# Kernel optimization log

Hardware: AMD Instinct MI355X
Metric: run time of the kernel (lower is better)

## Reference

```python
import jax, jax.numpy as jnp
import numpy as np

N = 100000            # number of pose-graph nodes (keyframes)
E = 2000000           # number of edges (last one is the 'key' edge)
KEY_EDGE_WEIGHT = 0.1 # default key_edge_weight in forward
_EPS2 = 1e-8          # small-angle threshold on squared norms
_TINY = 1e-12

# quaternion layout follows pypose: [x, y, z, w]; SE3 7-vec is [t(3), q(4)]

def _quat_to_mat(q):
    x, y, z, w = q[..., 0], q[..., 1], q[..., 2], q[..., 3]
    xx, yy, zz = x * x, y * y, z * z
    xy, xz, yz = x * y, x * z, y * z
    wx, wy, wz = w * x, w * y, w * z
    R = jnp.stack([
        jnp.stack([1 - 2 * (yy + zz), 2 * (xy - wz), 2 * (xz + wy)], -1),
        jnp.stack([2 * (xy + wz), 1 - 2 * (xx + zz), 2 * (yz - wx)], -1),
        jnp.stack([2 * (xz - wy), 2 * (yz + wx), 1 - 2 * (xx + yy)], -1),
    ], -2)
    return R  # [...,3,3]

def _mat_to_tq(M):
    """mat2SE3: [...,4,4] -> (t [...,3], q [...,4] xyzw). Branchless copysign method."""
    R = M[..., :3, :3]
    t = M[..., :3, 3]
    m00, m11, m22 = R[..., 0, 0], R[..., 1, 1], R[..., 2, 2]
    qw = 0.5 * jnp.sqrt(jnp.clip(1 + m00 + m11 + m22, _TINY))
    sx = jnp.where(R[..., 2, 1] - R[..., 1, 2] >= 0, 1.0, -1.0)
    sy = jnp.where(R[..., 0, 2] - R[..., 2, 0] >= 0, 1.0, -1.0)
    sz = jnp.where(R[..., 1, 0] - R[..., 0, 1] >= 0, 1.0, -1.0)
    qx = sx * 0.5 * jnp.sqrt(jnp.clip(1 + m00 - m11 - m22, _TINY))
    qy = sy * 0.5 * jnp.sqrt(jnp.clip(1 - m00 + m11 - m22, _TINY))
    qz = sz * 0.5 * jnp.sqrt(jnp.clip(1 - m00 - m11 + m22, _TINY))
    return t, jnp.stack([qx, qy, qz, qw], -1)

def _qmul(q1, q2):
    v1, w1 = q1[..., :3], q1[..., 3:]
    v2, w2 = q2[..., :3], q2[..., 3:]
    w = w1 * w2 - jnp.sum(v1 * v2, -1, keepdims=True)
    v = w1 * v2 + w2 * v1 + jnp.cross(v1, v2)
    return jnp.concatenate([v, w], -1)

def _qrot(q, v):
    qv, w = q[..., :3], q[..., 3:]
    return v + 2.0 * jnp.cross(qv, jnp.cross(qv, v) + w * v)

def _so3_log(q):
    """unit quaternion -> rotation vector phi [...,3]."""
    s = jnp.where(q[..., 3:] < 0, -1.0, 1.0)  # canonical hemisphere (w>=0)
    v, w = s * q[..., :3], (s * q[..., 3:])[..., 0]
    n2 = jnp.sum(v * v, -1)
    n = jnp.sqrt(jnp.clip(n2, _TINY))
    big = 2.0 * jnp.arctan2(n, w) / n
    small = 2.0 / w - 2.0 * n2 / (3.0 * w ** 3)
    scale = jnp.where(n2 > _EPS2, big, small)
    return scale[..., None] * v

def _se3_log(t, q):
    """SE3 Log map -> [tau(3), phi(3)] (pypose se3 ordering)."""
    phi = _so3_log(q)
    th2 = jnp.sum(phi * phi, -1)
    th = jnp.sqrt(jnp.clip(th2, _TINY))
    half = 0.5 * th
    sin_half = jnp.where(th2 > _EPS2, jnp.sin(half), 1.0)
    coef_big = (1.0 - half * jnp.cos(half) / sin_half) / jnp.clip(th2, _TINY)
    coef = jnp.where(th2 > _EPS2, coef_big, 1.0 / 12.0 + th2 / 720.0)
    pxt = jnp.cross(phi, t)
    tau = t - 0.5 * pxt + coef[..., None] * jnp.cross(phi, pxt)
    return jnp.concatenate([tau, phi], -1)

def setup_inputs() -> dict:
    key = jax.random.key(0)
    k1, k2, k3, k4, k5 = jax.random.split(key, 5)
    # node SE3 params: random unit quats + translations -> [N,7]
    qn = jax.random.normal(k1, (N, 4), jnp.float32)
    qn = qn / jnp.linalg.norm(qn, axis=-1, keepdims=True)
    tn = jax.random.normal(k2, (N, 3), jnp.float32)
    nodes = jnp.concatenate([tn, qn], -1)
    edges = jax.random.randint(k3, (E, 2), 0, N, dtype=jnp.int64)
    # measurement poses as valid 4x4 SE3 matrices [E,4,4]
    qe = jax.random.normal(k4, (E, 4), jnp.float32)
    qe = qe / jnp.linalg.norm(qe, axis=-1, keepdims=True)
    te = jax.random.normal(k5, (E, 3), jnp.float32)
    top = jnp.concatenate([_quat_to_mat(qe), te[..., None]], -1)   # [E,3,4]
    bottom = jnp.broadcast_to(jnp.array([0.0, 0.0, 0.0, 1.0], jnp.float32), (E, 1, 4))
    poses = jnp.concatenate([top, bottom], -2)
    return {"nodes": nodes, "poses": poses, "edges": edges}

def reference(nodes, poses, edges):
    # nodes_all = cat([poses_SE3[0:1] (frozen), nodes[1:]])
    nodes_all = jnp.concatenate([jax.lax.stop_gradient(nodes[:1]), nodes[1:]], 0)
    n1 = nodes_all[edges[:, 0]]
    n2 = nodes_all[edges[:, 1]]
    t1, q1 = n1[:, :3], n1[:, 3:]
    t2, q2 = n2[:, :3], n2[:, 3:]
    # rel = node1.Inv() @ node2
    q1i = jnp.concatenate([-q1[:, :3], q1[:, 3:]], -1)
    t12 = _qrot(q1i, t2 - t1)
    q12 = _qmul(q1i, q2)
    # error = mat2SE3(poses) @ rel
    tp, qp = _mat_to_tq(poses)
    te_ = tp + _qrot(qp, t12)
    qe_ = _qmul(qp, q12)
    err = _se3_log(te_, qe_)  # [E,6]
    # last edge is the key edge, scaled by key_edge_weight (same math as the
    # original's split-then-concat, done with one vectorized pass + row weight)
    w = jnp.concatenate([jnp.ones((E - 1,), err.dtype),
                         jnp.full((1,), KEY_EDGE_WEIGHT, err.dtype)])
    return err * w[:, None]
```

## Files before the change

kernel.cpp:

```cpp
#include <hip/hip_runtime.h>

#define K_EPS2 1e-8f
#define K_TINY 1e-12f
#define KEY_EDGE_WEIGHT 0.1f

__device__ __forceinline__ float3 f3(float x, float y, float z) { return make_float3(x, y, z); }
__device__ __forceinline__ float3 add3(float3 a, float3 b) { return f3(a.x + b.x, a.y + b.y, a.z + b.z); }
__device__ __forceinline__ float3 sub3(float3 a, float3 b) { return f3(a.x - b.x, a.y - b.y, a.z - b.z); }
__device__ __forceinline__ float3 scl3(float s, float3 a) { return f3(s * a.x, s * a.y, s * a.z); }
__device__ __forceinline__ float dot3(float3 a, float3 b) { return a.x * b.x + a.y * b.y + a.z * b.z; }
__device__ __forceinline__ float3 cross3(float3 a, float3 b) {
    return f3(a.y * b.z - a.z * b.y,
              a.z * b.x - a.x * b.z,
              a.x * b.y - a.y * b.x);
}

__device__ __forceinline__ float3 qrot(float3 qv, float qw, float3 v) {
    float3 t = add3(cross3(qv, v), scl3(qw, v));
    return add3(v, scl3(2.0f, cross3(qv, t)));
}

__device__ __forceinline__ void qmul(float3 v1, float w1, float3 v2, float w2,
                                     float3* v, float* w) {
    *w = w1 * w2 - dot3(v1, v2);
    *v = add3(add3(scl3(w1, v2), scl3(w2, v1)), cross3(v1, v2));
}

__global__ __launch_bounds__(256) void PoseGraph_kernel(
    const float* __restrict__ nodes,
    const float* __restrict__ poses,
    const int*   __restrict__ edges,
    float*       __restrict__ out,
    int E) {
    int e = blockIdx.x * blockDim.x + threadIdx.x;
    if (e >= E) return;

    int2 ij = *(const int2*)(edges + (size_t)2 * e);

    const float* pn1 = nodes + (size_t)ij.x * 7;
    const float* pn2 = nodes + (size_t)ij.y * 7;
    float3 t1  = f3(pn1[0], pn1[1], pn1[2]);
    float3 q1v = f3(pn1[3], pn1[4], pn1[5]);
    float  q1w = pn1[6];
    float3 t2  = f3(pn2[0], pn2[1], pn2[2]);
    float3 q2v = f3(pn2[3], pn2[4], pn2[5]);
    float  q2w = pn2[6];

    float3 q1iv = f3(-q1v.x, -q1v.y, -q1v.z);
    float3 t12 = qrot(q1iv, q1w, sub3(t2, t1));
    float3 q12v; float q12w;
    qmul(q1iv, q1w, q2v, q2w, &q12v, &q12w);

    const float4* p4 = (const float4*)(poses + (size_t)e * 16);
    float4 r0 = p4[0];
    float4 r1 = p4[1];
    float4 r2 = p4[2];
    float m00 = r0.x, m01 = r0.y, m02 = r0.z;
    float m10 = r1.x, m11 = r1.y, m12 = r1.z;
    float m20 = r2.x, m21 = r2.y, m22 = r2.z;
    float3 tp = f3(r0.w, r1.w, r2.w);

    float qpw = 0.5f * sqrtf(fmaxf(1.0f + m00 + m11 + m22, K_TINY));
    float qpx = ((m21 - m12 >= 0.0f) ? 0.5f : -0.5f) * sqrtf(fmaxf(1.0f + m00 - m11 - m22, K_TINY));
    float qpy = ((m02 - m20 >= 0.0f) ? 0.5f : -0.5f) * sqrtf(fmaxf(1.0f - m00 + m11 - m22, K_TINY));
    float qpz = ((m10 - m01 >= 0.0f) ? 0.5f : -0.5f) * sqrtf(fmaxf(1.0f - m00 - m11 + m22, K_TINY));
    float3 qpv = f3(qpx, qpy, qpz);

    float3 te = add3(tp, qrot(qpv, qpw, t12));
    float3 qev; float qew;
    qmul(qpv, qpw, q12v, q12w, &qev, &qew);

    float s = (qew < 0.0f) ? -1.0f : 1.0f;
    float3 v = scl3(s, qev);
    float w = s * qew;
    float nn2 = dot3(v, v);
    float scale;
    if (nn2 > K_EPS2) {
        float n = sqrtf(nn2);
        scale = 2.0f * atan2f(n, w) / n;
    } else {
        scale = 2.0f / w - 2.0f * nn2 / (3.0f * w * w * w);
    }
    float3 phi = scl3(scale, v);

    float th2 = dot3(phi, phi);
    float coef;
    if (th2 > K_EPS2) {
        float th = sqrtf(th2);
        float half = 0.5f * th;
        float sh = sinf(half);
        float ch = cosf(half);
        coef = (1.0f - half * ch / sh) / th2;
    } else {
        coef = 1.0f / 12.0f + th2 / 720.0f;
    }
    float3 pxt = cross3(phi, te);
    float3 tau = add3(sub3(te, scl3(0.5f, pxt)), scl3(coef, cross3(phi, pxt)));

    float wgt = (e == E - 1) ? KEY_EDGE_WEIGHT : 1.0f;

    float* o = out + (size_t)e * 6;
    *(float2*)(o + 0) = make_float2(tau.x * wgt, tau.y * wgt);
    *(float2*)(o + 2) = make_float2(tau.z * wgt, phi.x * wgt);
    *(float2*)(o + 4) = make_float2(phi.y * wgt, phi.z * wgt);
}

extern "C" void kernel_launch(void* const* d_in, const int* in_sizes, int n_in,
                              void* d_out, int out_size, void* d_ws, size_t ws_size,
                              hipStream_t stream) {
    const float* nodes = (const float*)d_in[0];
    const float* poses = (const float*)d_in[1];
    const int*   edges = (const int*)d_in[2];
    float* out = (float*)d_out;

    int E = in_sizes[2] / 2;
    int threads = 256;
    int blocks = (E + threads - 1) / threads;
    PoseGraph_kernel<<<blocks, threads, 0, stream>>>(nodes, poses, edges, out, E);
}
```

Before: 53.48 us.

## Repack node poses to 32-byte aligned rows and use nontemporal streaming accesses

Adds a pre-pass kernel that copies the 7-float node array into an 8-float padded workspace, so each gathered node can be read with two aligned 16-byte loads instead of seven scalar loads. Edge indices and pose matrices are now read, and outputs written, with nontemporal hints so streaming data does not evict the reused node table from cache. The cost is an extra kernel launch and a pass over the nodes each call. The packed path only runs when the workspace is large enough; otherwise the original layout is used.

Result: slower. 71.46 us (+33.6%).

```diff
diff --git a/kernel.cpp b/kernel.cpp
--- a/kernel.cpp
+++ b/kernel.cpp
@@ -3,6 +3,10 @@
 #define K_EPS2 1e-8f
 #define K_TINY 1e-12f
 #define KEY_EDGE_WEIGHT 0.1f
+
+typedef float  vf4 __attribute__((ext_vector_type(4)));
+typedef float  vf2 __attribute__((ext_vector_type(2)));
+typedef int    vi2 __attribute__((ext_vector_type(2)));
 
 __device__ __forceinline__ float3 f3(float x, float y, float z) { return make_float3(x, y, z); }
 __device__ __forceinline__ float3 add3(float3 a, float3 b) { return f3(a.x + b.x, a.y + b.y, a.z + b.z); }
@@ -26,6 +30,19 @@
     *v = add3(add3(scl3(w1, v2), scl3(w2, v1)), cross3(v1, v2));
 }
 
+__global__ __launch_bounds__(256) void pack_nodes_kernel(
+    const float* __restrict__ nodes, float* __restrict__ packed, int N) {
+    int i = blockIdx.x * blockDim.x + threadIdx.x;
+    if (i >= N) return;
+    const float* p = nodes + (size_t)7 * i;
+    vf4 a = { p[0], p[1], p[2], p[3] };
+    vf4 b = { p[4], p[5], p[6], 0.0f };
+    vf4* o = (vf4*)(packed + (size_t)8 * i);
+    o[0] = a;
+    o[1] = b;
+}
+
+template <bool PACKED>
 __global__ __launch_bounds__(256) void PoseGraph_kernel(
     const float* __restrict__ nodes,
     const float* __restrict__ poses,
@@ -35,26 +52,42 @@
     int e = blockIdx.x * blockDim.x + threadIdx.x;
     if (e >= E) return;
 
-    int2 ij = *(const int2*)(edges + (size_t)2 * e);
+    vi2 ij = __builtin_nontemporal_load((const vi2*)(edges + (size_t)2 * e));
 
-    const float* pn1 = nodes + (size_t)ij.x * 7;
-    const float* pn2 = nodes + (size_t)ij.y * 7;
-    float3 t1  = f3(pn1[0], pn1[1], pn1[2]);
-    float3 q1v = f3(pn1[3], pn1[4], pn1[5]);
-    float  q1w = pn1[6];
-    float3 t2  = f3(pn2[0], pn2[1], pn2[2]);
-    float3 q2v = f3(pn2[3], pn2[4], pn2[5]);
-    float  q2w = pn2[6];
+    float3 t1, q1v, t2, q2v;
+    float q1w, q2w;
+    if (PACKED) {
+        const vf4* pa = (const vf4*)(nodes + (size_t)8 * ij.x);
+        const vf4* pb = (const vf4*)(nodes + (size_t)8 * ij.y);
+        vf4 a0 = pa[0], a1 = pa[1];
+        vf4 b0 = pb[0], b1 = pb[1];
+        t1  = f3(a0.x, a0.y, a0.z);
+        q1v = f3(a0.w, a1.x, a1.y);
+        q1w = a1.z;
+        t2  = f3(b0.x, b0.y, b0.z);
+        q2v = f3(b0.w, b1.x, b1.y);
+        q2w = b1.z;
+    } else {
+        const float* pa = nodes + (size_t)7 * ij.x;
+        const float* pb = nodes + (size_t)7 * ij.y;
+        t1  = f3(pa[0], pa[1], pa[2]);
+        q1v = f3(pa[3], pa[4], pa[5]);
+        q1w = pa[6];
+        t2  = f3(pb[0], pb[1], pb[2]);
+        q2v = f3(pb[3], pb[4], pb[5]);
+        q2w = pb[6];
+    }
+
+    const vf4* p4 = (const vf4*)(poses + (size_t)e * 16);
+    vf4 r0 = __builtin_nontemporal_load(p4 + 0);
+    vf4 r1 = __builtin_nontemporal_load(p4 + 1);
+    vf4 r2 = __builtin_nontemporal_load(p4 + 2);
 
     float3 q1iv = f3(-q1v.x, -q1v.y, -q1v.z);
     float3 t12 = qrot(q1iv, q1w, sub3(t2, t1));
     float3 q12v; float q12w;
     qmul(q1iv, q1w, q2v, q2w, &q12v, &q12w);
 
-    const float4* p4 = (const float4*)(poses + (size_t)e * 16);
-    float4 r0 = p4[0];
-    float4 r1 = p4[1];
-    float4 r2 = p4[2];
     float m00 = r0.x, m01 = r0.y, m02 = r0.z;
     float m10 = r1.x, m11 = r1.y, m12 = r1.z;
     float m20 = r2.x, m21 = r2.y, m22 = r2.z;
@@ -99,10 +132,13 @@
 
     float wgt = (e == E - 1) ? KEY_EDGE_WEIGHT : 1.0f;
 
-    float* o = out + (size_t)e * 6;
-    *(float2*)(o + 0) = make_float2(tau.x * wgt, tau.y * wgt);
-    *(float2*)(o + 2) = make_float2(tau.z * wgt, phi.x * wgt);
-    *(float2*)(o + 4) = make_float2(phi.y * wgt, phi.z * wgt);
+    float* o = out + (size_t)6 * e;
+    vf2 o0 = { tau.x * wgt, tau.y * wgt };
+    vf2 o1 = { tau.z * wgt, phi.x * wgt };
+    vf2 o2 = { phi.y * wgt, phi.z * wgt };
+    __builtin_nontemporal_store(o0, (vf2*)(o + 0));
+    __builtin_nontemporal_store(o1, (vf2*)(o + 2));
+    __builtin_nontemporal_store(o2, (vf2*)(o + 4));
 }
 
 extern "C" void kernel_launch(void* const* d_in, const int* in_sizes, int n_in,
@@ -113,8 +149,18 @@
     const int*   edges = (const int*)d_in[2];
     float* out = (float*)d_out;
 
+    int N = in_sizes[0] / 7;
     int E = in_sizes[2] / 2;
     int threads = 256;
-    int blocks = (E + threads - 1) / threads;
-    PoseGraph_kernel<<<blocks, threads, 0, stream>>>(nodes, poses, edges, out, E);
+    int eblocks = (E + threads - 1) / threads;
+
+    size_t packed_bytes = (size_t)N * 8 * sizeof(float);
+    if (ws_size >= packed_bytes) {
+        float* packed = (float*)d_ws;
+        int nblocks = (N + threads - 1) / threads;
+        pack_nodes_kernel<<<nblocks, threads, 0, stream>>>(nodes, packed, N);
+        PoseGraph_kernel<true><<<eblocks, threads, 0, stream>>>(packed, poses, edges, out, E);
+    } else {
+        PoseGraph_kernel<false><<<eblocks, threads, 0, stream>>>(nodes, poses, edges, out, E);
+    }
 }
```
